# Optimization experiments

Measured on AMD Instinct MI355X. Metric: run time of the kernel, lower is better.

## Reference

```python
import jax, jax.numpy as jnp
import numpy as np

B, S, D = 32, 1024, 1024
H = 16            # attention heads
T = 8             # num_tasks (probe tokens)
E = 8             # num_experts
K = 2             # top_k
HID = 4 * D       # expert hidden dim
EPS = 1e-5


def setup_inputs() -> dict:
    key = jax.random.key(0)
    ks = jax.random.split(key, 12)
    sd = 1.0 / np.sqrt(D)
    inp = {
        "x": jax.random.normal(ks[0], (B, S, D), jnp.float32),
        "probe": jax.random.normal(ks[1], (1, T, D), jnp.float32) * 0.02,
        "in_proj_w": jax.random.normal(ks[2], (3 * D, D), jnp.float32) * sd,
        "in_proj_b": jnp.zeros((3 * D,), jnp.float32),
        "out_proj_w": jax.random.normal(ks[3], (D, D), jnp.float32) * sd,
        "out_proj_b": jnp.zeros((D,), jnp.float32),
        "ln_gamma": jnp.ones((D,), jnp.float32),
        "ln_beta": jnp.zeros((D,), jnp.float32),
        "gate_w": jax.random.normal(ks[4], (T, D, E), jnp.float32) * sd,  # per-task gate (task-aware)
        "w1": jax.random.normal(ks[5], (E, D, HID), jnp.float32) * sd,
        "b1": jnp.zeros((E, HID), jnp.float32),
        "w2": jax.random.normal(ks[6], (E, HID, D), jnp.float32) / np.sqrt(HID),
        "b2": jnp.zeros((E, D), jnp.float32),
    }
    return inp


def reference(x, probe, in_proj_w, in_proj_b, out_proj_w, out_proj_b,
              ln_gamma, ln_beta, gate_w, w1, b1, w2, b2):
    b, s, d = x.shape
    t = probe.shape[1]
    dh = d // H
    # --- multihead cross attention: query = probe, key/value = x ---
    wq, wk, wv = in_proj_w[:d], in_proj_w[d:2 * d], in_proj_w[2 * d:]
    bq, bk, bv = in_proj_b[:d], in_proj_b[d:2 * d], in_proj_b[2 * d:]
    q = jnp.broadcast_to(probe, (b, t, d)) @ wq.T + bq           # [B,T,D]
    k = x @ wk.T + bk                                            # [B,S,D]
    v = x @ wv.T + bv
    q = q.reshape(b, t, H, dh).transpose(0, 2, 1, 3)             # bhtd
    k = k.reshape(b, s, H, dh).transpose(0, 2, 1, 3)             # bhsd
    v = v.reshape(b, s, H, dh).transpose(0, 2, 1, 3)
    scores = jnp.einsum('bhtd,bhsd->bhts', q, k) / np.sqrt(dh)
    attn = jax.nn.softmax(scores, axis=-1)                       # [B,H,T,S]
    ctx = jnp.einsum('bhts,bhsd->bhtd', attn, v)
    ctx = ctx.transpose(0, 2, 1, 3).reshape(b, t, d)
    attn_out = ctx @ out_proj_w.T + out_proj_b                   # [B,T,D]
    attn_weights = attn.mean(axis=1)                             # torch avg over heads
    # --- layernorm ---
    mu = attn_out.mean(-1, keepdims=True)
    var = attn_out.var(-1, keepdims=True)
    y = (attn_out - mu) * jax.lax.rsqrt(var + EPS) * ln_gamma + ln_beta
    # --- task-aware MoE: per-task gate, top-k routing ---
    logits = jnp.einsum('btd,tde->bte', y, gate_w)               # [B,T,E]
    probs = jax.nn.softmax(logits, axis=-1)
    tok = y.reshape(b * t, d)
    p = probs.reshape(b * t, E)
    topv, topi = jax.lax.top_k(p, K)                             # [N,K]
    wgt = topv / topv.sum(-1, keepdims=True)
    gates = jnp.zeros((b * t, E), y.dtype).at[jnp.arange(b * t)[:, None], topi].set(wgt)
    # all experts on all tokens (N=B*T is small); grouped GEMM form
    h = jax.nn.gelu(jnp.einsum('nd,edh->enh', tok, w1) + b1[:, None, :], approximate=False)
    eo = jnp.einsum('enh,ehd->end', h, w2) + b2[:, None, :]      # [E,N,D]
    moe_out = jnp.einsum('ne,end->nd', gates, eo).reshape(b, t, d)
    # load-balancing aux loss
    dispatch = (jax.nn.one_hot(topi, E, dtype=y.dtype)).sum(1)   # [N,E] 0/1
    f = dispatch.mean(0)
    P = p.mean(0)
    moe_loss = E * jnp.sum(f * P)
    final = attn_out + moe_out
    return final, moe_loss, attn_weights
```

## Files before the change

### kernel.cpp

```cpp
#include <hip/hip_runtime.h>
#include <hip/hip_bf16.h>
#include <math.h>


using bf16x8  = __attribute__((ext_vector_type(8))) short;
using f32x4   = __attribute__((ext_vector_type(4))) float;
using short4v = __attribute__((ext_vector_type(4))) short;

__device__ inline short f2bf(float f) {
  unsigned u = __builtin_bit_cast(unsigned, f);
  u = (u + 0x7fffu + ((u >> 16) & 1u)) >> 16;
  return (short)u;
}
__device__ inline int bswz(int k, int n) {
  return (((k >> 3) ^ ((n >> 2) & 3)) << 3) | (k & 7);
}

static constexpr long OFF_Q       = 0;
static constexpr long OFF_QWB     = 8192;
static constexpr long OFF_QB      = 73728;
static constexpr long OFF_PSUM    = 73856;
static constexpr long OFF_FCNT    = 73864;
static constexpr long OFF_GATES   = 73872;
static constexpr long OFF_CTX     = 75920;
static constexpr long OFF_ATTNOUT = 338064;
static constexpr long OFF_EO      = 600208;
static constexpr long OFF_CTXP    = 2697360;
static constexpr long OFF_AOP     = 3745936;
static constexpr long OFF_SCORES  = 4794512;
static constexpr long OFF_AXP     = 8988816;
static constexpr long OFF_YB      = 17377424;
static constexpr long OFF_HB      = 17508496;

__global__ __launch_bounds__(256) void compute_q_k(const float* __restrict__ probe,
                                                   const float* __restrict__ in_w,
                                                   const float* __restrict__ in_b,
                                                   float* __restrict__ q) {
  int wid = threadIdx.x >> 6, lane = threadIdx.x & 63;
  int idx = blockIdx.x * 4 + wid;
  int t = idx >> 10, d = idx & 1023;
  const float* pr = probe + (long)t * 1024;
  const float* wr = in_w + (long)d * 1024;
  float s = 0.f;
  for (int k = lane * 4; k < 1024; k += 256) {
    float4 a = *(const float4*)&pr[k];
    float4 b = *(const float4*)&wr[k];
    s += a.x * b.x + a.y * b.y + a.z * b.z + a.w * b.w;
  }
  for (int o = 32; o; o >>= 1) s += __shfl_xor(s, o);
  if (!lane) q[idx] = s + in_b[d];
}

__global__ __launch_bounds__(256) void compute_qw_k(const float* __restrict__ q,
                                                    const float* __restrict__ in_w,
                                                    const float* __restrict__ in_b,
                                                    short* __restrict__ qwb,
                                                    float* __restrict__ qb) {
  const int h = blockIdx.y;
  const int tid = threadIdx.x;
  const int d = blockIdx.x * 256 + tid;
  __shared__ float qh[8][64];
  if (tid < 64) {
#pragma unroll
    for (int t = 0; t < 8; ++t) qh[t][tid] = q[t * 1024 + h * 64 + tid] * 0.125f;
  }
  __syncthreads();
  const float* wk = in_w + 1048576 + (long)h * 64 * 1024;
  float acc[8];
#pragma unroll
  for (int t = 0; t < 8; ++t) acc[t] = 0.f;
  for (int j = 0; j < 64; ++j) {
    float w = wk[(long)j * 1024 + d];
#pragma unroll
    for (int t = 0; t < 8; ++t) acc[t] += qh[t][j] * w;
  }
#pragma unroll
  for (int t = 0; t < 8; ++t) qwb[(long)(h * 8 + t) * 1024 + d] = f2bf(acc[t]);
  if (blockIdx.x == 0 && tid < 8) {
    float s = 0.f;
    for (int j = 0; j < 64; ++j) s += qh[tid][j] * in_b[1024 + h * 64 + j];
    qb[h * 8 + tid] = s;
  }
}

__global__ __launch_bounds__(512)
void gemm_sc(const short* __restrict__ qwb, const float* __restrict__ xp,
             float* __restrict__ scores) {
  const int b = blockIdx.z;
  const int n0 = blockIdx.x * 64;
  const float* B = xp + (long)b * 1048576;
  float* C = scores + (long)b * 131072;
  const int tid = threadIdx.x;
  __shared__ short As[128][40], Bs[64][40];

  f32x4 acc[2][2];
#pragma unroll
  for (int i = 0; i < 2; ++i)
#pragma unroll
    for (int j = 0; j < 2; ++j)
#pragma unroll
      for (int qq = 0; qq < 4; ++qq) acc[i][j][qq] = 0.f;

  const int wid = tid >> 6, lane = tid & 63;
  const int wm = wid & 3, wn = wid >> 2;
  const int r = lane & 15, kg = (lane >> 4) * 8;
  const int am = tid >> 2, ak8 = (tid & 3) * 8;
  const int bn = tid >> 3, bk4 = (tid & 7) * 4;

  bf16x8 ra0, ra1;
  float4 rb0, rb1;
  auto loadA = [&](int k0) { return *(const bf16x8*)&qwb[(long)am * 1024 + k0 + ak8]; };
  auto loadB = [&](int k0) { return *(const float4*)&B[(long)(n0 + bn) * 1024 + k0 + bk4]; };
  auto store = [&](bf16x8 ra, float4 rb) {
    *(bf16x8*)&As[am][ak8] = ra;
    short4v s;
    s.x = f2bf(rb.x); s.y = f2bf(rb.y); s.z = f2bf(rb.z); s.w = f2bf(rb.w);
    *(short4v*)&Bs[bn][bk4] = s;
  };
  auto compute = [&]() {
    bf16x8 af[2], bf_[2];
#pragma unroll
    for (int i = 0; i < 2; ++i) af[i] = *(const bf16x8*)&As[wm * 32 + i * 16 + r][kg];
#pragma unroll
    for (int j = 0; j < 2; ++j) bf_[j] = *(const bf16x8*)&Bs[wn * 32 + j * 16 + r][kg];
#pragma unroll
    for (int i = 0; i < 2; ++i)
#pragma unroll
      for (int j = 0; j < 2; ++j)
        acc[i][j] = __builtin_amdgcn_mfma_f32_16x16x32_bf16(af[i], bf_[j], acc[i][j], 0, 0, 0);
  };

  ra0 = loadA(0);  rb0 = loadB(0);
  ra1 = loadA(32); rb1 = loadB(32);
  for (int k0 = 0; k0 < 1024; k0 += 64) {
    store(ra0, rb0);
    __syncthreads();
    if (k0 + 64 < 1024) { ra0 = loadA(k0 + 64); rb0 = loadB(k0 + 64); }
    compute();
    __syncthreads();
    store(ra1, rb1);
    __syncthreads();
    if (k0 + 96 < 1024) { ra1 = loadA(k0 + 96); rb1 = loadB(k0 + 96); }
    compute();
    __syncthreads();
  }

  const int q4 = (lane >> 4) * 4;
#pragma unroll
  for (int i = 0; i < 2; ++i)
#pragma unroll
    for (int j = 0; j < 2; ++j) {
      int gn = n0 + wn * 32 + j * 16 + r;
#pragma unroll
      for (int qq = 0; qq < 4; ++qq) {
        int m = wm * 32 + i * 16 + q4 + qq;
        C[(long)m * 1024 + gn] = acc[i][j][qq];
      }
    }
}

template<int WM, int WN, int KS, bool AKB, bool BTRANS, int APL, int EPI, bool DEEP2>
__global__ __launch_bounds__(WM * WN * 64)
void gemm_ss(const float* __restrict__ Ap, const float* __restrict__ Bp,
             const float* __restrict__ kbias, float* __restrict__ Cp,
             int lda, int ldb, int K,
             long zA, long zA2, long zB, long zC, long ZKC, int ldc) {
  constexpr int BM = WM * 64, BN = WN * 64, BK = 32, NT = WM * WN * 64, PK = 40;
  constexpr int LA = BM * BK / (NT * 4), LB = BN * BK / (NT * 4);
  constexpr int F4 = BN / 4;
  const int z = blockIdx.z, zo = z / KS, kc = z % KS;
  const float* A = Ap + zA * zo + (long)kc * K;
  const float* B = BTRANS ? (Bp + zB * zo + (long)kc * K * ldb)
                          : (Bp + zB * zo + (long)kc * K);
  const float* kb = kbias + (long)kc * K;
  float* C = Cp + zC * zo + ZKC * kc;
  const int tid = threadIdx.x;
  const int m0 = blockIdx.y * BM, n0 = blockIdx.x * BN;
  __shared__ short Ah[BM][PK], Al[BM][PK], Bh[BN][PK], Bl[BN][PK];

  f32x4 acc[4][4];
#pragma unroll
  for (int i = 0; i < 4; ++i)
#pragma unroll
    for (int j = 0; j < 4; ++j)
#pragma unroll
      for (int qq = 0; qq < 4; ++qq) acc[i][j][qq] = 0.f;

  const int wid = tid >> 6, lane = tid & 63;
  const int wm = wid % WM, wn = wid / WM;
  const int r = lane & 15, kg = (lane >> 4) * 8;

  auto loadT = [&](int k0, float4* ra, float4* rb) {
#pragma unroll
    for (int i = 0; i < LA; ++i) {
      int f = tid + i * NT;
      int m = f >> 3, k4 = (f & 7) * 4;
      long ofs = (long)(m0 + m) * lda + k0 + k4;
      ra[i] = *(const float4*)&A[ofs];
#pragma unroll
      for (int p = 1; p < APL; ++p) {
        float4 v2 = *(const float4*)&A[ofs + zA2 * p];
        ra[i].x += v2.x; ra[i].y += v2.y; ra[i].z += v2.z; ra[i].w += v2.w;
      }
      if (AKB) {
        float4 kv = *(const float4*)&kb[k0 + k4];
        ra[i].x += kv.x; ra[i].y += kv.y; ra[i].z += kv.z; ra[i].w += kv.w;
      }
    }
#pragma unroll
    for (int i = 0; i < LB; ++i) {
      int f = tid + i * NT;
      if (BTRANS) {
        int k = f / F4, n4 = (f % F4) * 4;
        rb[i] = *(const float4*)&B[(long)(k0 + k) * ldb + n0 + n4];
      } else {
        int n = f >> 3, k4 = (f & 7) * 4;
        rb[i] = *(const float4*)&B[(long)(n0 + n) * ldb + k0 + k4];
      }
    }
  };

  auto storeT = [&](float4* ra, float4* rb) {
#pragma unroll
    for (int i = 0; i < LA; ++i) {
      int f = tid + i * NT;
      int m = f >> 3, k4 = (f & 7) * 4;
      short4v h, l;
      float vv[4] = {ra[i].x, ra[i].y, ra[i].z, ra[i].w};
#pragma unroll
      for (int j = 0; j < 4; ++j) {
        unsigned u = __builtin_bit_cast(unsigned, vv[j]);
        h[j] = (short)(u >> 16);
        l[j] = f2bf(vv[j] - __builtin_bit_cast(float, u & 0xFFFF0000u));
      }
      *(short4v*)&Ah[m][k4] = h;
      *(short4v*)&Al[m][k4] = l;
    }
#pragma unroll
    for (int i = 0; i < LB; ++i) {
      int f = tid + i * NT;
      float vv[4] = {rb[i].x, rb[i].y, rb[i].z, rb[i].w};
      if (BTRANS) {
        int k = f / F4, n4 = (f % F4) * 4;
        int col = bswz(k, n4);
#pragma unroll
        for (int j = 0; j < 4; ++j) {
          unsigned u = __builtin_bit_cast(unsigned, vv[j]);
          Bh[n4 + j][col] = (short)(u >> 16);
          Bl[n4 + j][col] = f2bf(vv[j] - __builtin_bit_cast(float, u & 0xFFFF0000u));
        }
      } else {
        int n = f >> 3, k4 = (f & 7) * 4;
        short4v h, l;
#pragma unroll
        for (int j = 0; j < 4; ++j) {
          unsigned u = __builtin_bit_cast(unsigned, vv[j]);
          h[j] = (short)(u >> 16);
          l[j] = f2bf(vv[j] - __builtin_bit_cast(float, u & 0xFFFF0000u));
        }
        *(short4v*)&Bh[n][k4] = h;
        *(short4v*)&Bl[n][k4] = l;
      }
    }
  };

  auto compute = [&]() {
    bf16x8 ah[4], al[4], bh[4], bl[4];
#pragma unroll
    for (int i = 0; i < 4; ++i) {
      ah[i] = *(const bf16x8*)&Ah[wm * 64 + i * 16 + r][kg];
      al[i] = *(const bf16x8*)&Al[wm * 64 + i * 16 + r][kg];
    }
#pragma unroll
    for (int j = 0; j < 4; ++j) {
      int brow = wn * 64 + j * 16 + r;
      int bcol = BTRANS ? bswz(kg, brow) : kg;
      bh[j] = *(const bf16x8*)&Bh[brow][bcol];
      bl[j] = *(const bf16x8*)&Bl[brow][bcol];
    }
#pragma unroll
    for (int i = 0; i < 4; ++i)
#pragma unroll
      for (int j = 0; j < 4; ++j) {
        acc[i][j] = __builtin_amdgcn_mfma_f32_16x16x32_bf16(ah[i], bh[j], acc[i][j], 0, 0, 0);
        acc[i][j] = __builtin_amdgcn_mfma_f32_16x16x32_bf16(ah[i], bl[j], acc[i][j], 0, 0, 0);
        acc[i][j] = __builtin_amdgcn_mfma_f32_16x16x32_bf16(al[i], bh[j], acc[i][j], 0, 0, 0);
      }
  };

  if constexpr (DEEP2) {
    float4 ra0[LA], rb0[LB], ra1[LA], rb1[LB];
    loadT(0, ra0, rb0);
    loadT(BK, ra1, rb1);
    for (int k0 = 0; k0 < K; k0 += 2 * BK) {
      storeT(ra0, rb0);
      __syncthreads();
      if (k0 + 2 * BK < K) loadT(k0 + 2 * BK, ra0, rb0);
      compute();
      __syncthreads();
      storeT(ra1, rb1);
      __syncthreads();
      if (k0 + 3 * BK < K) loadT(k0 + 3 * BK, ra1, rb1);
      compute();
      __syncthreads();
    }
  } else {
    float4 ra[LA], rb[LB];
    loadT(0, ra, rb);
    for (int k0 = 0; k0 < K; k0 += BK) {
      storeT(ra, rb);
      __syncthreads();
      if (k0 + BK < K) loadT(k0 + BK, ra, rb);
      compute();
      __syncthreads();
    }
  }

  const int q4 = (lane >> 4) * 4;
#pragma unroll
  for (int i = 0; i < 4; ++i) {
    int gmb = m0 + wm * 64 + i * 16 + q4;
#pragma unroll
    for (int j = 0; j < 4; ++j) {
      int gn = n0 + wn * 64 + j * 16 + r;
#pragma unroll
      for (int qq = 0; qq < 4; ++qq) {
        float v = acc[i][j][qq];
        int m = gmb + qq;
        if constexpr (EPI == 0) {
          C[(long)m * ldc + gn] = v;
        } else {
          C[(long)(m >> 3) * 262144 + (long)(m & 7) * 1024 + gn] = v;
        }
      }
    }
  }
}

template<int WM, int WN, int KS, int EPI>
__global__ __launch_bounds__(WM * WN * 64)
void gemm_bw(const short* __restrict__ Ap, const float* __restrict__ Bp,
             const float* __restrict__ biasp, void* __restrict__ Cp,
             int lda, int ldb, int K, long zA, long zB, long zBias, long zC, int ldc) {
  constexpr int BM = WM * 64, BN = WN * 64, BK = 32, NT = WM * WN * 64, PK = 40;
  constexpr int LA = BM * BK / (NT * 8), LB = BN * BK / (NT * 4);
  constexpr int F4 = BN / 4;
  const int z = blockIdx.z, zo = z / KS, kc = z % KS;
  const short* A = Ap + zA * zo + (long)kc * K;
  const float* B = Bp + zB * zo + (long)kc * K * ldb;
  const float* bias = biasp + zBias * zo;
  const int tid = threadIdx.x;
  const int m0 = blockIdx.y * BM, n0 = blockIdx.x * BN;
  __shared__ short As[BM][PK], Bs[BN][PK];

  f32x4 acc[4][4];
#pragma unroll
  for (int i = 0; i < 4; ++i)
#pragma unroll
    for (int j = 0; j < 4; ++j)
#pragma unroll
      for (int qq = 0; qq < 4; ++qq) acc[i][j][qq] = 0.f;

  const int wid = tid >> 6, lane = tid & 63;
  const int wm = wid % WM, wn = wid / WM;
  const int r = lane & 15, kg = (lane >> 4) * 8;

  auto loadT = [&](int k0, bf16x8* ra, float4* rb) {
#pragma unroll
    for (int i = 0; i < LA; ++i) {
      int f = tid + i * NT;
      int m = f >> 2, k8 = (f & 3) * 8;
      ra[i] = *(const bf16x8*)&A[(long)(m0 + m) * lda + k0 + k8];
    }
#pragma unroll
    for (int i = 0; i < LB; ++i) {
      int f = tid + i * NT;
      int k = f / F4, n4 = (f % F4) * 4;
      rb[i] = *(const float4*)&B[(long)(k0 + k) * ldb + n0 + n4];
    }
  };

  auto storeT = [&](bf16x8* ra, float4* rb) {
#pragma unroll
    for (int i = 0; i < LA; ++i) {
      int f = tid + i * NT;
      int m = f >> 2, k8 = (f & 3) * 8;
      *(bf16x8*)&As[m][k8] = ra[i];
    }
#pragma unroll
    for (int i = 0; i < LB; ++i) {
      int f = tid + i * NT;
      int k = f / F4, n4 = (f % F4) * 4;
      int col = bswz(k, n4);
      Bs[n4 + 0][col] = f2bf(rb[i].x);
      Bs[n4 + 1][col] = f2bf(rb[i].y);
      Bs[n4 + 2][col] = f2bf(rb[i].z);
      Bs[n4 + 3][col] = f2bf(rb[i].w);
    }
  };

  auto compute = [&]() {
    bf16x8 af[4], bfr[4];
#pragma unroll
    for (int i = 0; i < 4; ++i) af[i] = *(const bf16x8*)&As[wm * 64 + i * 16 + r][kg];
#pragma unroll
    for (int j = 0; j < 4; ++j) {
      int brow = wn * 64 + j * 16 + r;
      bfr[j] = *(const bf16x8*)&Bs[brow][bswz(kg, brow)];
    }
#pragma unroll
    for (int i = 0; i < 4; ++i)
#pragma unroll
      for (int j = 0; j < 4; ++j)
        acc[i][j] = __builtin_amdgcn_mfma_f32_16x16x32_bf16(af[i], bfr[j], acc[i][j], 0, 0, 0);
  };

  bf16x8 ra0[LA], ra1[LA];
  float4 rb0[LB], rb1[LB];
  loadT(0, ra0, rb0);
  loadT(BK, ra1, rb1);
  for (int k0 = 0; k0 < K; k0 += 2 * BK) {
    storeT(ra0, rb0);
    __syncthreads();
    if (k0 + 2 * BK < K) loadT(k0 + 2 * BK, ra0, rb0);
    compute();
    __syncthreads();
    storeT(ra1, rb1);
    __syncthreads();
    if (k0 + 3 * BK < K) loadT(k0 + 3 * BK, ra1, rb1);
    compute();
    __syncthreads();
  }

  const int q4 = (lane >> 4) * 4;
#pragma unroll
  for (int i = 0; i < 4; ++i) {
    int gmb = m0 + wm * 64 + i * 16 + q4;
#pragma unroll
    for (int j = 0; j < 4; ++j) {
      int gn = n0 + wn * 64 + j * 16 + r;
#pragma unroll
      for (int qq = 0; qq < 4; ++qq) {
        float v = acc[i][j][qq];
        int m = gmb + qq;
        if constexpr (EPI == 2) {
          float u = v + bias[gn];
          u = 0.5f * u * (1.0f + erff(u * 0.70710678118654752f));
          ((short*)Cp + zC * zo)[(long)m * ldc + gn] = f2bf(u);
        } else {
          atomicAdd(&((float*)Cp + zC * zo)[(long)m * ldc + gn], v);
        }
      }
    }
  }
}

__global__ __launch_bounds__(256) void reduce4_k(const float* __restrict__ p,
                                                 float* __restrict__ out) {
  int i = (blockIdx.x * 256 + threadIdx.x) * 4;
  float4 a = *(const float4*)&p[i];
  float4 b = *(const float4*)&p[i + 262144];
  float4 c = *(const float4*)&p[i + 524288];
  float4 d = *(const float4*)&p[i + 786432];
  float4 o;
  o.x = a.x + b.x + c.x + d.x;
  o.y = a.y + b.y + c.y + d.y;
  o.z = a.z + b.z + c.z + d.z;
  o.w = a.w + b.w + c.w + d.w;
  *(float4*)&out[i] = o;
}

__global__ __launch_bounds__(256) void softmax_k(float* __restrict__ scores,
                                                 const float* __restrict__ qb) {
  long row = blockIdx.x;
  float bias = qb[(int)(row & 127)];
  float* p = scores + row * 1024;
  int tid = threadIdx.x;
  int wid = tid >> 6, lane = tid & 63;
  float v[4];
  float mx = -1e30f;
#pragma unroll
  for (int i = 0; i < 4; ++i) {
    v[i] = p[tid + i * 256] + bias;
    mx = fmaxf(mx, v[i]);
  }
  for (int o = 32; o; o >>= 1) mx = fmaxf(mx, __shfl_xor(mx, o));
  __shared__ float sm[4];
  __shared__ float ss[4];
  if (!lane) sm[wid] = mx;
  __syncthreads();
  mx = fmaxf(fmaxf(sm[0], sm[1]), fmaxf(sm[2], sm[3]));
  float s = 0.f;
#pragma unroll
  for (int i = 0; i < 4; ++i) { v[i] = expf(v[i] - mx); s += v[i]; }
  for (int o = 32; o; o >>= 1) s += __shfl_xor(s, o);
  if (!lane) ss[wid] = s;
  __syncthreads();
  s = ss[0] + ss[1] + ss[2] + ss[3];
  float inv = 1.0f / s;
#pragma unroll
  for (int i = 0; i < 4; ++i) p[tid + i * 256] = v[i] * inv;
}

__global__ __launch_bounds__(256) void attnw_k(const float* __restrict__ attn,
                                               float* __restrict__ outw) {
  int idx = blockIdx.x * 256 + threadIdx.x;
  int b = idx >> 13;
  int r = idx & 8191;
  int t = r >> 10, s = r & 1023;
  const float* p = attn + (long)b * 131072 + (long)t * 1024 + s;
  float acc = 0.f;
#pragma unroll
  for (int h = 0; h < 16; ++h) acc += p[(long)h * 8192];
  outw[idx] = acc * (1.0f / 16.0f);
}

__global__ __launch_bounds__(256) void ln_gate_k(const float* __restrict__ aop,
                                                 const float* __restrict__ out_b,
                                                 const float* __restrict__ gamma,
                                                 const float* __restrict__ beta,
                                                 const float* __restrict__ gate_w,
                                                 float* __restrict__ attn_out,
                                                 short* __restrict__ yb,
                                                 float* __restrict__ gates,
                                                 float* __restrict__ Psum,
                                                 float* __restrict__ fcnt) {
  int row = blockIdx.x;
  int t = row & 7;
  int tid = threadIdx.x;
  int wid = tid >> 6, lane = tid & 63;
  const float* xr = aop + (long)row * 1024;
  float vals[4];
  float s = 0.f, sq = 0.f;
#pragma unroll
  for (int i = 0; i < 4; ++i) {
    int d = tid + i * 256;
    float v = xr[d] + xr[d + 262144] + xr[d + 524288] + xr[d + 786432] + out_b[d];
    attn_out[(long)row * 1024 + d] = v;
    vals[i] = v;
    s += v;
    sq += v * v;
  }
  for (int o = 32; o; o >>= 1) { s += __shfl_xor(s, o); sq += __shfl_xor(sq, o); }
  __shared__ float rs[4], rss[4];
  if (!lane) { rs[wid] = s; rss[wid] = sq; }
  __syncthreads();
  s = rs[0] + rs[1] + rs[2] + rs[3];
  sq = rss[0] + rss[1] + rss[2] + rss[3];
  float mu = s * (1.0f / 1024.0f);
  float var = sq * (1.0f / 1024.0f) - mu * mu;
  float rstd = rsqrtf(var + 1e-5f);
  __shared__ float yrow[1024];
#pragma unroll
  for (int i = 0; i < 4; ++i) {
    int d = tid + i * 256;
    float yv = (vals[i] - mu) * rstd * gamma[d] + beta[d];
    yb[(long)row * 1024 + d] = f2bf(yv);
    yrow[d] = yv;
  }
  __syncthreads();
  int e = tid & 7;
  int g = tid >> 3;
  float acc = 0.f;
  const float* gw = gate_w + (long)t * 8192;
  for (int d = g; d < 1024; d += 32) acc += yrow[d] * gw[d * 8 + e];
  __shared__ float part[256];
  __shared__ float lsh[8];
  part[tid] = acc;
  __syncthreads();
  if (tid < 8) {
    float l = 0.f;
    for (int gg = 0; gg < 32; ++gg) l += part[gg * 8 + tid];
    lsh[tid] = l;
  }
  __syncthreads();
  if (tid == 0) {
    float p[8];
    float mx = -1e30f;
    for (int k = 0; k < 8; ++k) mx = fmaxf(mx, lsh[k]);
    float sum = 0.f;
    for (int k = 0; k < 8; ++k) { p[k] = expf(lsh[k] - mx); sum += p[k]; }
    float inv = 1.0f / sum;
    for (int k = 0; k < 8; ++k) p[k] *= inv;
    int i0 = 0;
    for (int k = 1; k < 8; ++k) if (p[k] > p[i0]) i0 = k;
    int i1 = -1;
    for (int k = 0; k < 8; ++k) if (k != i0 && (i1 < 0 || p[k] > p[i1])) i1 = k;
    float tot = p[i0] + p[i1];
    for (int k = 0; k < 8; ++k)
      gates[(long)row * 8 + k] = (k == i0) ? p[i0] / tot : (k == i1) ? p[i1] / tot : 0.f;
    for (int k = 0; k < 8; ++k) atomicAdd(&Psum[k], p[k]);
    atomicAdd(&fcnt[i0], 1.0f);
    atomicAdd(&fcnt[i1], 1.0f);
  }
}

__global__ __launch_bounds__(256) void combine_k(const float* __restrict__ attn_out,
                                                 const float* __restrict__ eo,
                                                 const float* __restrict__ b2,
                                                 const float* __restrict__ gates,
                                                 float* __restrict__ outp) {
  int idx = blockIdx.x * 256 + threadIdx.x;
  int n = idx >> 10, d = idx & 1023;
  float v = attn_out[idx];
  const float* g = gates + (long)n * 8;
#pragma unroll
  for (int e = 0; e < 8; ++e) {
    float ge = g[e];
    if (ge != 0.f) v += ge * (eo[(long)e * 262144 + idx] + b2[e * 1024 + d]);
  }
  outp[idx] = v;
}

__global__ void loss_k(const float* __restrict__ Psum, const float* __restrict__ fcnt,
                       float* __restrict__ out) {
  if (threadIdx.x == 0) {
    float l = 0.f;
    for (int e = 0; e < 8; ++e) l += (fcnt[e] * (1.0f / 256.0f)) * (Psum[e] * (1.0f / 256.0f));
    out[0] = 8.0f * l;
  }
}

extern "C" void kernel_launch(void* const* d_in, const int* in_sizes, int n_in,
                              void* d_out, int out_size, void* d_ws, size_t ws_size,
                              hipStream_t stream) {
  const float* x      = (const float*)d_in[0];
  const float* probe  = (const float*)d_in[1];
  const float* in_w   = (const float*)d_in[2];
  const float* in_b   = (const float*)d_in[3];
  const float* out_w  = (const float*)d_in[4];
  const float* out_b  = (const float*)d_in[5];
  const float* gamma  = (const float*)d_in[6];
  const float* beta   = (const float*)d_in[7];
  const float* gate_w = (const float*)d_in[8];
  const float* w1     = (const float*)d_in[9];
  const float* b1     = (const float*)d_in[10];
  const float* w2     = (const float*)d_in[11];
  const float* b2     = (const float*)d_in[12];

  float* ws = (float*)d_ws;
  float* q        = ws + OFF_Q;
  short* qwb      = (short*)(ws + OFF_QWB);
  float* qb       = ws + OFF_QB;
  float* Psum     = ws + OFF_PSUM;
  float* fcnt     = ws + OFF_FCNT;
  float* gates    = ws + OFF_GATES;
  float* ctx      = ws + OFF_CTX;
  float* attn_out = ws + OFF_ATTNOUT;
  float* eo       = ws + OFF_EO;
  float* ctxp     = ws + OFF_CTXP;
  float* aop      = ws + OFF_AOP;
  float* scores   = ws + OFF_SCORES;
  float* axp      = ws + OFF_AXP;
  short* yb       = (short*)(ws + OFF_YB);
  short* hb       = (short*)(ws + OFF_HB);

  float* out_final = (float*)d_out;
  float* out_loss  = out_final + 262144;
  float* out_attnw = out_loss + 1;

  hipMemsetAsync(ws + OFF_PSUM, 0, 16 * sizeof(float), stream);
  hipMemsetAsync(eo, 0, 2097152 * sizeof(float), stream);

  compute_q_k<<<2048, 256, 0, stream>>>(probe, in_w, in_b, q);
  compute_qw_k<<<dim3(4, 16, 1), 256, 0, stream>>>(q, in_w, in_b, qwb, qb);

  gemm_sc<<<dim3(16, 1, 32), 512, 0, stream>>>(qwb, x, scores);

  softmax_k<<<4096, 256, 0, stream>>>(scores, qb);
  attnw_k<<<1024, 256, 0, stream>>>(scores, out_attnw);

  gemm_ss<2, 2, 2, false, true, 1, 4, true><<<dim3(8, 1, 64), 256, 0, stream>>>(
      scores, x, qb , axp, 1024, 1024, 512,
      131072L, 0L, 1048576L, 8192L, 4194304L, 1024);

  gemm_ss<1, 1, 4, false, false, 2, 0, false><<<dim3(1, 4, 64), 64, 0, stream>>>(
      axp, in_w + 2097152, qb , ctxp, 1024, 1024, 256,
      262144L, 4194304L, 65536L, 64L, 262144L, 1024);
  reduce4_k<<<256, 256, 0, stream>>>(ctxp, ctx);

  gemm_ss<1, 1, 4, true, false, 1, 0, false><<<dim3(16, 4, 4), 64, 0, stream>>>(
      ctx, out_w, in_b + 2048, aop, 1024, 1024, 256,
      0L, 0L, 0L, 0L, 262144L, 1024);

  ln_gate_k<<<256, 256, 0, stream>>>(aop, out_b, gamma, beta, gate_w, attn_out,
                                     yb, gates, Psum, fcnt);

  gemm_bw<2, 2, 1, 2><<<dim3(32, 2, 8), 256, 0, stream>>>(
      yb, w1, b1, hb, 1024, 4096, 1024, 0L, 4194304L, 4096L, 1048576L, 4096);

  gemm_bw<2, 2, 4, 5><<<dim3(8, 2, 32), 256, 0, stream>>>(
      hb, w2, b2 , eo, 4096, 1024, 1024, 1048576L, 4194304L, 0L, 262144L, 1024);

  combine_k<<<1024, 256, 0, stream>>>(attn_out, eo, b2, gates, out_final);
  loss_k<<<1, 64, 0, stream>>>(Psum, fcnt, out_loss);
}
```

Measured before the change: 380.1 us.

## Rework GEMM k-loops with single-stage register prefetch and LDS double buffering

Replaces the two-register-set unrolled k-loops in the score, split-scale and bw GEMMs with a single prefetch set per tile, using raw s_barrier plus explicit lgkmcnt waits instead of __syncthreads. The bw GEMM gains double-buffered LDS, so one barrier per tile suffices and the store for the next tile overlaps the compute on the current one. The aim is lower barrier overhead and register pressure. In exchange each prefetch has less time to hide global latency, and the bw kernel uses twice the LDS, which may reduce occupancy.

```diff
diff --git a/kernel.cpp b/kernel.cpp
--- a/kernel.cpp
+++ b/kernel.cpp
@@ -15,6 +15,9 @@
 __device__ inline int bswz(int k, int n) {
   return (((k >> 3) ^ ((n >> 2) & 3)) << 3) | (k & 7);
 }
+
+#define LGKM0() asm volatile("s_waitcnt lgkmcnt(0)" ::: "memory")
+#define RAWBAR() do { __builtin_amdgcn_s_barrier(); __builtin_amdgcn_sched_barrier(0); } while (0)
 
 static constexpr long OFF_Q       = 0;
 static constexpr long OFF_QWB     = 8192;
@@ -107,11 +110,13 @@
   const int am = tid >> 2, ak8 = (tid & 3) * 8;
   const int bn = tid >> 3, bk4 = (tid & 7) * 4;
 
-  bf16x8 ra0, ra1;
-  float4 rb0, rb1;
-  auto loadA = [&](int k0) { return *(const bf16x8*)&qwb[(long)am * 1024 + k0 + ak8]; };
-  auto loadB = [&](int k0) { return *(const float4*)&B[(long)(n0 + bn) * 1024 + k0 + bk4]; };
-  auto store = [&](bf16x8 ra, float4 rb) {
+  bf16x8 ra;
+  float4 rb;
+  auto loadT = [&](int k0) {
+    ra = *(const bf16x8*)&qwb[(long)am * 1024 + k0 + ak8];
+    rb = *(const float4*)&B[(long)(n0 + bn) * 1024 + k0 + bk4];
+  };
+  auto storeT = [&]() {
     *(bf16x8*)&As[am][ak8] = ra;
     short4v s;
     s.x = f2bf(rb.x); s.y = f2bf(rb.y); s.z = f2bf(rb.z); s.w = f2bf(rb.w);
@@ -130,19 +135,19 @@
         acc[i][j] = __builtin_amdgcn_mfma_f32_16x16x32_bf16(af[i], bf_[j], acc[i][j], 0, 0, 0);
   };
 
-  ra0 = loadA(0);  rb0 = loadB(0);
-  ra1 = loadA(32); rb1 = loadB(32);
-  for (int k0 = 0; k0 < 1024; k0 += 64) {
-    store(ra0, rb0);
-    __syncthreads();
-    if (k0 + 64 < 1024) { ra0 = loadA(k0 + 64); rb0 = loadB(k0 + 64); }
+  constexpr int NTILES = 32;
+  loadT(0);
+  storeT();
+  loadT(32);
+  LGKM0(); RAWBAR();
+  for (int t = 0; t < NTILES; ++t) {
     compute();
-    __syncthreads();
-    store(ra1, rb1);
-    __syncthreads();
-    if (k0 + 96 < 1024) { ra1 = loadA(k0 + 96); rb1 = loadB(k0 + 96); }
-    compute();
-    __syncthreads();
+    if (t + 1 < NTILES) {
+      LGKM0(); RAWBAR();
+      storeT();
+      if (t + 2 < NTILES) loadT((t + 2) * 32);
+      LGKM0(); RAWBAR();
+    }
   }
 
   const int q4 = (lane >> 4) * 4;
@@ -159,7 +164,7 @@
     }
 }
 
-template<int WM, int WN, int KS, bool AKB, bool BTRANS, int APL, int EPI, bool DEEP2>
+template<int WM, int WN, int KS, bool AKB, bool BTRANS, int APL, int EPI>
 __global__ __launch_bounds__(WM * WN * 64)
 void gemm_ss(const float* __restrict__ Ap, const float* __restrict__ Bp,
              const float* __restrict__ kbias, float* __restrict__ Cp,
@@ -190,7 +195,9 @@
   const int wm = wid % WM, wn = wid / WM;
   const int r = lane & 15, kg = (lane >> 4) * 8;
 
-  auto loadT = [&](int k0, float4* ra, float4* rb) {
+  float4 ra[LA], rb[LB];
+
+  auto loadT = [&](int k0) {
 #pragma unroll
     for (int i = 0; i < LA; ++i) {
       int f = tid + i * NT;
@@ -220,7 +227,7 @@
     }
   };
 
-  auto storeT = [&](float4* ra, float4* rb) {
+  auto storeT = [&]() {
 #pragma unroll
     for (int i = 0; i < LA; ++i) {
       int f = tid + i * NT;
@@ -288,31 +295,18 @@
       }
   };
 
-  if constexpr (DEEP2) {
-    float4 ra0[LA], rb0[LB], ra1[LA], rb1[LB];
-    loadT(0, ra0, rb0);
-    loadT(BK, ra1, rb1);
-    for (int k0 = 0; k0 < K; k0 += 2 * BK) {
-      storeT(ra0, rb0);
-      __syncthreads();
-      if (k0 + 2 * BK < K) loadT(k0 + 2 * BK, ra0, rb0);
-      compute();
-      __syncthreads();
-      storeT(ra1, rb1);
-      __syncthreads();
-      if (k0 + 3 * BK < K) loadT(k0 + 3 * BK, ra1, rb1);
-      compute();
-      __syncthreads();
-    }
-  } else {
-    float4 ra[LA], rb[LB];
-    loadT(0, ra, rb);
-    for (int k0 = 0; k0 < K; k0 += BK) {
-      storeT(ra, rb);
-      __syncthreads();
-      if (k0 + BK < K) loadT(k0 + BK, ra, rb);
-      compute();
-      __syncthreads();
+  const int NTILES = K / BK;
+  loadT(0);
+  storeT();
+  if (NTILES > 1) loadT(BK);
+  LGKM0(); RAWBAR();
+  for (int t = 0; t < NTILES; ++t) {
+    compute();
+    if (t + 1 < NTILES) {
+      LGKM0(); RAWBAR();
+      storeT();
+      if (t + 2 < NTILES) loadT((t + 2) * BK);
+      LGKM0(); RAWBAR();
     }
   }
 
@@ -351,7 +345,7 @@
   const float* bias = biasp + zBias * zo;
   const int tid = threadIdx.x;
   const int m0 = blockIdx.y * BM, n0 = blockIdx.x * BN;
-  __shared__ short As[BM][PK], Bs[BN][PK];
+  __shared__ short As[2][BM][PK], Bs[2][BN][PK];
 
   f32x4 acc[4][4];
 #pragma unroll
@@ -365,7 +359,10 @@
   const int wm = wid % WM, wn = wid / WM;
   const int r = lane & 15, kg = (lane >> 4) * 8;
 
-  auto loadT = [&](int k0, bf16x8* ra, float4* rb) {
+  bf16x8 ra[LA];
+  float4 rb[LB];
+
+  auto loadT = [&](int k0) {
 #pragma unroll
     for (int i = 0; i < LA; ++i) {
       int f = tid + i * NT;
@@ -380,33 +377,33 @@
     }
   };
 
-  auto storeT = [&](bf16x8* ra, float4* rb) {
+  auto storeT = [&](int bi) {
 #pragma unroll
     for (int i = 0; i < LA; ++i) {
       int f = tid + i * NT;
       int m = f >> 2, k8 = (f & 3) * 8;
-      *(bf16x8*)&As[m][k8] = ra[i];
+      *(bf16x8*)&As[bi][m][k8] = ra[i];
     }
 #pragma unroll
     for (int i = 0; i < LB; ++i) {
       int f = tid + i * NT;
       int k = f / F4, n4 = (f % F4) * 4;
       int col = bswz(k, n4);
-      Bs[n4 + 0][col] = f2bf(rb[i].x);
-      Bs[n4 + 1][col] = f2bf(rb[i].y);
-      Bs[n4 + 2][col] = f2bf(rb[i].z);
-      Bs[n4 + 3][col] = f2bf(rb[i].w);
-    }
-  };
-
-  auto compute = [&]() {
+      Bs[bi][n4 + 0][col] = f2bf(rb[i].x);
+      Bs[bi][n4 + 1][col] = f2bf(rb[i].y);
+      Bs[bi][n4 + 2][col] = f2bf(rb[i].z);
+      Bs[bi][n4 + 3][col] = f2bf(rb[i].w);
+    }
+  };
+
+  auto compute = [&](int bi) {
     bf16x8 af[4], bfr[4];
 #pragma unroll
-    for (int i = 0; i < 4; ++i) af[i] = *(const bf16x8*)&As[wm * 64 + i * 16 + r][kg];
+    for (int i = 0; i < 4; ++i) af[i] = *(const bf16x8*)&As[bi][wm * 64 + i * 16 + r][kg];
 #pragma unroll
     for (int j = 0; j < 4; ++j) {
       int brow = wn * 64 + j * 16 + r;
-      bfr[j] = *(const bf16x8*)&Bs[brow][bswz(kg, brow)];
+      bfr[j] = *(const bf16x8*)&Bs[bi][brow][bswz(kg, brow)];
     }
 #pragma unroll
     for (int i = 0; i < 4; ++i)
@@ -415,21 +412,18 @@
         acc[i][j] = __builtin_amdgcn_mfma_f32_16x16x32_bf16(af[i], bfr[j], acc[i][j], 0, 0, 0);
   };
 
-  bf16x8 ra0[LA], ra1[LA];
-  float4 rb0[LB], rb1[LB];
-  loadT(0, ra0, rb0);
-  loadT(BK, ra1, rb1);
-  for (int k0 = 0; k0 < K; k0 += 2 * BK) {
-    storeT(ra0, rb0);
-    __syncthreads();
-    if (k0 + 2 * BK < K) loadT(k0 + 2 * BK, ra0, rb0);
-    compute();
-    __syncthreads();
-    storeT(ra1, rb1);
-    __syncthreads();
-    if (k0 + 3 * BK < K) loadT(k0 + 3 * BK, ra1, rb1);
-    compute();
-    __syncthreads();
+  const int NTILES = K / BK;
+  loadT(0);
+  storeT(0);
+  if (NTILES > 1) loadT(BK);
+  LGKM0(); RAWBAR();
+  for (int t = 0; t < NTILES; ++t) {
+    compute(t & 1);
+    if (t + 1 < NTILES) {
+      storeT((t + 1) & 1);
+      if (t + 2 < NTILES) loadT((t + 2) * BK);
+      LGKM0(); RAWBAR();
+    }
   }
 
   const int q4 = (lane >> 4) * 4;
@@ -670,16 +664,16 @@
   softmax_k<<<4096, 256, 0, stream>>>(scores, qb);
   attnw_k<<<1024, 256, 0, stream>>>(scores, out_attnw);
 
-  gemm_ss<2, 2, 2, false, true, 1, 4, true><<<dim3(8, 1, 64), 256, 0, stream>>>(
+  gemm_ss<2, 2, 2, false, true, 1, 4><<<dim3(8, 1, 64), 256, 0, stream>>>(
       scores, x, qb , axp, 1024, 1024, 512,
       131072L, 0L, 1048576L, 8192L, 4194304L, 1024);
 
-  gemm_ss<1, 1, 4, false, false, 2, 0, false><<<dim3(1, 4, 64), 64, 0, stream>>>(
+  gemm_ss<1, 1, 4, false, false, 2, 0><<<dim3(1, 4, 64), 64, 0, stream>>>(
       axp, in_w + 2097152, qb , ctxp, 1024, 1024, 256,
       262144L, 4194304L, 65536L, 64L, 262144L, 1024);
   reduce4_k<<<256, 256, 0, stream>>>(ctxp, ctx);
 
-  gemm_ss<1, 1, 4, true, false, 1, 0, false><<<dim3(16, 4, 4), 64, 0, stream>>>(
+  gemm_ss<1, 1, 4, true, false, 1, 0><<<dim3(16, 4, 4), 64, 0, stream>>>(
       ctx, out_w, in_b + 2048, aop, 1024, 1024, 256,
       0L, 0L, 0L, 0L, 262144L, 1024);
 
```

Measured after the change: 364.8 us. -4.0%, faster.
